# Kernel tuning notes

Hardware: AMD Instinct MI355X
Metric: run time of the kernel (lower is better)

The kernel has to match this reference:

```python
import jax, jax.numpy as jnp
import numpy as np

H = 16  # num heads
DH = 64  # head dim


def setup_inputs() -> dict:
    key = jax.random.key(0)
    ks = jax.random.split(key, 9)
    d = 1024
    s = 0.02
    return {
        "hidden_states": jax.random.normal(ks[0], (16, 1024, d), jnp.float32),
        "Wq": jax.random.normal(ks[1], (d, d), jnp.float32) * s,
        "bq": jax.random.normal(ks[2], (d,), jnp.float32) * s,
        "Wk": jax.random.normal(ks[3], (d, d), jnp.float32) * s,
        "bk": jax.random.normal(ks[4], (d,), jnp.float32) * s,
        "Wv": jax.random.normal(ks[5], (d, d), jnp.float32) * s,
        "bv": jax.random.normal(ks[6], (d,), jnp.float32) * s,
        "Wo": jax.random.normal(ks[7], (d, d), jnp.float32) * s,
        "bo": jax.random.normal(ks[8], (d,), jnp.float32) * s,
    }


def _heads(x):
    b, s, _ = x.shape
    return x.reshape(b, s, H, DH).transpose(0, 2, 1, 3)  # [B,H,S,Dh]


def reference(hidden_states, Wq, bq, Wk, bk, Wv, bv, Wo, bo):
    # torch nn.Linear: y = x @ W.T + b; weights here are [out, in]
    q = _heads(hidden_states @ Wq.T + bq)
    k = _heads(hidden_states @ Wk.T + bk)
    v = _heads(hidden_states @ Wv.T + bv)
    scores = jnp.einsum("bhqd,bhkd->bhqk", q, k) / jnp.sqrt(jnp.float32(DH))
    probs = jax.nn.softmax(scores, axis=-1)
    ctx = jnp.einsum("bhqk,bhkd->bhqd", probs, v)
    b, _, s, _ = ctx.shape
    ctx = ctx.transpose(0, 2, 1, 3).reshape(b, s, H * DH)
    out = ctx @ Wo.T + bo
    # module returns (attention_output, weights=None); return array only
    return out
```

## Files before the change

### kernel.cpp

```cpp
#include <hip/hip_runtime.h>
#include <hip/hip_bf16.h>
#include <stdint.h>


typedef short bf16x8 __attribute__((ext_vector_type(8)));
typedef float f32x4 __attribute__((ext_vector_type(4)));
typedef float f32x16 __attribute__((ext_vector_type(16)));
typedef unsigned short ushort_t;
typedef ushort_t us8 __attribute__((ext_vector_type(8)));

__device__ __forceinline__ ushort_t f2b(float f) {
    unsigned x;
    __builtin_memcpy(&x, &f, 4);
    unsigned r = (x + 0x7fffu + ((x >> 16) & 1u)) >> 16;
    return (ushort_t)r;
}

__device__ __forceinline__ void glds16(const void* g, void* l) {
    __builtin_amdgcn_global_load_lds(
        (const __attribute__((address_space(1))) void*)g,
        (__attribute__((address_space(3))) void*)l, 16, 0, 0);
}

#define MFMA16(a, b, c) __builtin_amdgcn_mfma_f32_16x16x32_bf16((a), (b), (c), 0, 0, 0)
#define MFMA32(a, b, c) __builtin_amdgcn_mfma_f32_32x32x16_bf16((a), (b), (c), 0, 0, 0)

__global__ __launch_bounds__(256, 8) void cvt4_kernel(
    const float* __restrict__ s0, const float* __restrict__ s1,
    const float* __restrict__ s2, const float* __restrict__ s3,
    ushort_t* __restrict__ d0, ushort_t* __restrict__ d1,
    ushort_t* __restrict__ d2, ushort_t* __restrict__ d3, int n8)
{
    const float* in = (blockIdx.y == 0) ? s0 : (blockIdx.y == 1) ? s1
                       : (blockIdx.y == 2) ? s2 : s3;
    ushort_t* out = (blockIdx.y == 0) ? d0 : (blockIdx.y == 1) ? d1
                       : (blockIdx.y == 2) ? d2 : d3;
    int i = blockIdx.x * 256 + threadIdx.x;
    if (i >= n8) return;
    const float4* p = (const float4*)in + (size_t)i * 2;
    float4 a = p[0], b = p[1];
    us8 v;
    v[0] = f2b(a.x); v[1] = f2b(a.y); v[2] = f2b(a.z); v[3] = f2b(a.w);
    v[4] = f2b(b.x); v[5] = f2b(b.y); v[6] = f2b(b.z); v[7] = f2b(b.w);
    *((us8*)out + i) = v;
}

__global__ __launch_bounds__(256, 8) void cvt1_kernel(
    const float* __restrict__ in, ushort_t* __restrict__ out, int n8)
{
    int i = blockIdx.x * 256 + threadIdx.x;
    if (i >= n8) return;
    const float4* p = (const float4*)in + (size_t)i * 2;
    float4 a = p[0], b = p[1];
    us8 v;
    v[0] = f2b(a.x); v[1] = f2b(a.y); v[2] = f2b(a.z); v[3] = f2b(a.w);
    v[4] = f2b(b.x); v[5] = f2b(b.y); v[6] = f2b(b.z); v[7] = f2b(b.w);
    *((us8*)out + i) = v;
}

template <bool OUTF>
__global__ __launch_bounds__(512) void gemm256_kernel(
    const ushort_t* __restrict__ A,
    const ushort_t* __restrict__ W0, const ushort_t* __restrict__ W1, const ushort_t* __restrict__ W2,
    const float* __restrict__ b0, const float* __restrict__ b1, const float* __restrict__ b2,
    void* __restrict__ C0, void* __restrict__ C1, void* __restrict__ C2,
    float s0, float s1, float s2, int N, int K)
{
    const ushort_t* W = (blockIdx.z == 0) ? W0 : ((blockIdx.z == 1) ? W1 : W2);
    const float* bias = (blockIdx.z == 0) ? b0 : ((blockIdx.z == 1) ? b1 : b2);
    void* C = (blockIdx.z == 0) ? C0 : ((blockIdx.z == 1) ? C1 : C2);
    const float scale = (blockIdx.z == 0) ? s0 : ((blockIdx.z == 1) ? s1 : s2);

    __shared__ ushort_t lds[2][4][256 * 32];

    const int tid = threadIdx.x;
    const int lane = tid & 63;
    const int wave = tid >> 6;
    const int wr = wave >> 2;
    const int wc = wave & 3;
    const int r32 = lane & 31;
    const int g = lane >> 5;

    const int gx = gridDim.x;
    const int flat = blockIdx.y * gx + blockIdx.x;
    const int cpx = (gx * gridDim.y) >> 3;
    const int swz = (flat & 7) * cpx + (flat >> 3);
    const int bm = (swz % gx) * 256;
    const int bn = (swz / gx) * 256;

    const ushort_t* Ag = A + (size_t)bm * K;
    const ushort_t* Bg = W + (size_t)bn * K;

    const int q0 = tid, q1 = 512 + tid;
    const int sr0 = q0 >> 2, sc0 = (((q0 & 3) - (sr0 >> 1)) & 3) * 8;
    const int sr1 = q1 >> 2, sc1 = (((q1 & 3) - (sr1 >> 1)) & 3) * 8;

#define STG(gbase, kcol, dst) do { \
    glds16((gbase) + (size_t)sr0 * K + (kcol) + sc0, (dst) + q0 * 8); \
    glds16((gbase) + (size_t)sr1 * K + (kcol) + sc1, (dst) + q1 * 8); } while (0)

#define BARRIER() do { \
    __builtin_amdgcn_sched_barrier(0); \
    asm volatile("s_barrier" ::: "memory"); \
    __builtin_amdgcn_sched_barrier(0); } while (0)

#define VMCNT(n) asm volatile("s_waitcnt vmcnt(" #n ")" ::: "memory")

#define ROT(r, c) (((((c) + ((r) >> 1)) & 3)) * 8)

    f32x16 acc[4][2] = {};
    bf16x8 af[2][2], bfr[2][2];

#define LDA(buf, kh, mh) do { _Pragma("unroll") \
    for (int i = 0; i < 2; ++i) { _Pragma("unroll") \
        for (int t = 0; t < 2; ++t) { \
            int row = wr * 128 + ((mh) * 2 + i) * 32 + r32; \
            af[i][t] = *(const bf16x8*)(&lds[buf][kh][0] + row * 32 + ROT(row, 2 * t + g)); \
        } } } while (0)
#define LDB(buf, kh) do { _Pragma("unroll") \
    for (int ni = 0; ni < 2; ++ni) { _Pragma("unroll") \
        for (int t = 0; t < 2; ++t) { \
            int row = wc * 64 + ni * 32 + r32; \
            bfr[ni][t] = *(const bf16x8*)(&lds[buf][2 + (kh)][0] + row * 32 + ROT(row, 2 * t + g)); \
        } } } while (0)
#define MM(mh) do { __builtin_amdgcn_s_setprio(1); _Pragma("unroll") \
    for (int i = 0; i < 2; ++i) { _Pragma("unroll") \
        for (int ni = 0; ni < 2; ++ni) { \
            acc[(mh) * 2 + i][ni] = MFMA32(af[i][0], bfr[ni][0], acc[(mh) * 2 + i][ni]); \
            acc[(mh) * 2 + i][ni] = MFMA32(af[i][1], bfr[ni][1], acc[(mh) * 2 + i][ni]); \
        } } \
    __builtin_amdgcn_s_setprio(0); } while (0)

    STG(Ag, 0,  &lds[0][0][0]);
    STG(Bg, 0,  &lds[0][2][0]);
    STG(Ag, 32, &lds[0][1][0]);
    STG(Bg, 32, &lds[0][3][0]);
    STG(Bg, 64, &lds[1][2][0]);
    STG(Ag, 64, &lds[1][0][0]);
    VMCNT(4);
    BARRIER();

#pragma unroll 1
    for (int i = 0; i < 7; ++i) {
        const int t = 2 * i;
        const int kc1 = (t + 1) * 64, kc2 = (t + 2) * 64, kc3 = (t + 3) * 64;
        LDB(0, 0); LDA(0, 0, 0);
        STG(Bg, kc1 + 32, &lds[1][3][0]);
        BARRIER(); MM(0);
        LDA(0, 0, 1);
        STG(Ag, kc1 + 32, &lds[1][1][0]);
        VMCNT(8);
        BARRIER(); MM(1);
        LDB(0, 1); LDA(0, 1, 0);
        STG(Bg, kc2, &lds[0][2][0]);
        BARRIER(); MM(0);
        LDA(0, 1, 1);
        STG(Ag, kc2, &lds[0][0][0]);
        VMCNT(8);
        BARRIER(); MM(1);
        LDB(1, 0); LDA(1, 0, 0);
        STG(Bg, kc2 + 32, &lds[0][3][0]);
        BARRIER(); MM(0);
        LDA(1, 0, 1);
        STG(Ag, kc2 + 32, &lds[0][1][0]);
        VMCNT(8);
        BARRIER(); MM(1);
        LDB(1, 1); LDA(1, 1, 0);
        STG(Bg, kc3, &lds[1][2][0]);
        BARRIER(); MM(0);
        LDA(1, 1, 1);
        STG(Ag, kc3, &lds[1][0][0]);
        VMCNT(8);
        BARRIER(); MM(1);
    }

    {
        const int kc15 = 15 * 64;
        LDB(0, 0); LDA(0, 0, 0);
        STG(Bg, kc15 + 32, &lds[1][3][0]);
        BARRIER(); MM(0);
        LDA(0, 0, 1);
        STG(Ag, kc15 + 32, &lds[1][1][0]);
        VMCNT(8);
        BARRIER(); MM(1);
        LDB(0, 1); LDA(0, 1, 0);
        BARRIER(); MM(0);
        LDA(0, 1, 1);
        VMCNT(0);
        BARRIER(); MM(1);
        LDB(1, 0); LDA(1, 0, 0); MM(0);
        LDA(1, 0, 1); MM(1);
        LDB(1, 1); LDA(1, 1, 0); MM(0);
        LDA(1, 1, 1); MM(1);
    }

#pragma unroll
    for (int ni = 0; ni < 2; ++ni) {
        const int col = bn + wc * 64 + ni * 32 + r32;
        const float bv = bias[col];
#pragma unroll
        for (int mi = 0; mi < 4; ++mi) {
            const int rbase = bm + wr * 128 + mi * 32 + 4 * g;
#pragma unroll
            for (int reg = 0; reg < 16; ++reg) {
                const int row = rbase + (reg & 3) + 8 * (reg >> 2);
                float v = (acc[mi][ni][reg] + bv) * scale;
                if (OUTF)
                    ((float*)C)[(size_t)row * N + col] = v;
                else
                    ((ushort_t*)C)[(size_t)row * N + col] = f2b(v);
            }
        }
    }
#undef STG
#undef BARRIER
#undef VMCNT
#undef ROT
#undef LDA
#undef LDB
#undef MM
}

__global__ __launch_bounds__(256, 4) void transpose_v_kernel(
    const ushort_t* __restrict__ V, ushort_t* __restrict__ Vt)
{
    __shared__ ushort_t t[64 * 65];
    const int bh = blockIdx.x;
    const int st = blockIdx.y;
    const int b = bh >> 4, h = bh & 15;
    const int tid = threadIdx.x;

#pragma unroll
    for (int i = 0; i < 16; ++i) {
        int e = i * 256 + tid;
        int s = e >> 6, d = e & 63;
        t[s * 65 + d] = V[(size_t)(b * 1024 + st * 64 + s) * 1024 + h * 64 + d];
    }
    __syncthreads();
#pragma unroll
    for (int i = 0; i < 16; ++i) {
        int e = i * 256 + tid;
        int d = e >> 6, s = e & 63;
        Vt[(size_t)(bh * 64 + d) * 1024 + st * 64 + s] = t[s * 65 + d];
    }
}

__global__ __launch_bounds__(256, 2) void attn_kernel(
    const ushort_t* __restrict__ Q, const ushort_t* __restrict__ K,
    const ushort_t* __restrict__ Vt, ushort_t* __restrict__ ctx)
{
    __shared__ ushort_t Ks[2][64 * 64];
    __shared__ ushort_t Vs[2][64 * 64];
    __shared__ ushort_t Ps[4][32 * 72];

    const int bh = blockIdx.x;
    const int qt = blockIdx.y;
    const int b = bh >> 4, h = bh & 15;
    const int tid = threadIdx.x;
    const int lane = tid & 63;
    const int wave = tid >> 6;
    const int q = lane >> 4;
    const int ml = lane & 15;

    const int cid0 = tid;
    const int cid1 = 256 + tid;
    const int r0 = cid0 >> 3, sc0 = (cid0 & 7) ^ (r0 & 7);
    const int r1 = cid1 >> 3, sc1 = (cid1 & 7) ^ (r1 & 7);
    const ushort_t* Kbase = K + (size_t)(b * 1024) * 1024 + h * 64;
    const ushort_t* Vbase = Vt + (size_t)(bh * 64) * 1024;

    bf16x8 qf[2][2];
#pragma unroll
    for (int mg = 0; mg < 2; ++mg) {
        int row = b * 1024 + qt * 128 + wave * 32 + mg * 16 + ml;
        const ushort_t* qp = Q + (size_t)row * 1024 + h * 64;
        qf[mg][0] = *(const bf16x8*)(qp + q * 8);
        qf[mg][1] = *(const bf16x8*)(qp + 32 + q * 8);
    }

    bf16x8 ones;
#pragma unroll
    for (int i = 0; i < 8; ++i) ones[i] = (short)0x3F80;

    f32x4 o[2][4] = {};
    f32x4 ls[2] = {};
    ushort_t* Pw = Ps[wave];

    glds16(Kbase + (size_t)r0 * 1024 + sc0 * 8, Ks[0] + cid0 * 8);
    glds16(Vbase + (size_t)r0 * 1024 + sc0 * 8, Vs[0] + cid0 * 8);
    glds16(Kbase + (size_t)r1 * 1024 + sc1 * 8, Ks[0] + cid1 * 8);
    glds16(Vbase + (size_t)r1 * 1024 + sc1 * 8, Vs[0] + cid1 * 8);

    for (int kt = 0; kt < 16; ++kt) {
        const int cur = kt & 1, nxt = cur ^ 1;
        __syncthreads();
        if (kt + 1 < 16) {
            const ushort_t* Kn = Kbase + (size_t)(kt + 1) * 64 * 1024;
            const ushort_t* Vn = Vbase + (kt + 1) * 64;
            glds16(Kn + (size_t)r0 * 1024 + sc0 * 8, Ks[nxt] + cid0 * 8);
            glds16(Vn + (size_t)r0 * 1024 + sc0 * 8, Vs[nxt] + cid0 * 8);
            glds16(Kn + (size_t)r1 * 1024 + sc1 * 8, Ks[nxt] + cid1 * 8);
            glds16(Vn + (size_t)r1 * 1024 + sc1 * 8, Vs[nxt] + cid1 * 8);
        }
        const ushort_t* Kc = Ks[cur];
        const ushort_t* Vc = Vs[cur];

#pragma unroll
        for (int n = 0; n < 4; ++n) {
            int row = n * 16 + ml;
            int c0 = q ^ (row & 7);
            int c1 = (4 + q) ^ (row & 7);
            bf16x8 k0 = *(const bf16x8*)(Kc + row * 64 + c0 * 8);
            bf16x8 k1 = *(const bf16x8*)(Kc + row * 64 + c1 * 8);
#pragma unroll
            for (int mg = 0; mg < 2; ++mg) {
                f32x4 z = {};
                z = MFMA16(k0, qf[mg][0], z);
                z = MFMA16(k1, qf[mg][1], z);
                float p0 = __builtin_amdgcn_exp2f(z[0]);
                float p1 = __builtin_amdgcn_exp2f(z[1]);
                float p2 = __builtin_amdgcn_exp2f(z[2]);
                float p3 = __builtin_amdgcn_exp2f(z[3]);
                __hip_bfloat162 h01 = __float22bfloat162_rn(make_float2(p0, p1));
                __hip_bfloat162 h23 = __float22bfloat162_rn(make_float2(p2, p3));
                uint2 dd;
                __builtin_memcpy(&dd.x, &h01, 4);
                __builtin_memcpy(&dd.y, &h23, 4);
                *(uint2*)(Pw + (mg * 16 + ml) * 72 + n * 16 + q * 4) = dd;
            }
        }

#pragma unroll
        for (int mg = 0; mg < 2; ++mg) {
            bf16x8 pf0 = *(const bf16x8*)(Pw + (mg * 16 + ml) * 72 + q * 8);
            bf16x8 pf1 = *(const bf16x8*)(Pw + (mg * 16 + ml) * 72 + 32 + q * 8);
            ls[mg] = MFMA16(pf0, ones, ls[mg]);
            ls[mg] = MFMA16(pf1, ones, ls[mg]);
#pragma unroll
            for (int n = 0; n < 4; ++n) {
                int row = n * 16 + ml;
                int c0 = q ^ (row & 7);
                int c1 = (4 + q) ^ (row & 7);
                bf16x8 v0 = *(const bf16x8*)(Vc + row * 64 + c0 * 8);
                bf16x8 v1 = *(const bf16x8*)(Vc + row * 64 + c1 * 8);
                o[mg][n] = MFMA16(pf0, v0, o[mg][n]);
                o[mg][n] = MFMA16(pf1, v1, o[mg][n]);
            }
        }
    }

    const int orow_base = b * 1024 + qt * 128 + wave * 32;
#pragma unroll
    for (int mg = 0; mg < 2; ++mg) {
#pragma unroll
        for (int r = 0; r < 4; ++r) {
            float lv = 1.0f / ls[mg][r];
            int orow = orow_base + mg * 16 + q * 4 + r;
#pragma unroll
            for (int n = 0; n < 4; ++n) {
                ctx[(size_t)orow * 1024 + h * 64 + n * 16 + ml] =
                    f2b(o[mg][n][r] * lv);
            }
        }
    }
}

extern "C" void kernel_launch(void* const* d_in, const int* in_sizes, int n_in,
                              void* d_out, int out_size, void* d_ws, size_t ws_size,
                              hipStream_t stream)
{
    const float* X  = (const float*)d_in[0];
    const float* Wq = (const float*)d_in[1];
    const float* bq = (const float*)d_in[2];
    const float* Wk = (const float*)d_in[3];
    const float* bk = (const float*)d_in[4];
    const float* Wv = (const float*)d_in[5];
    const float* bv = (const float*)d_in[6];
    const float* Wo = (const float*)d_in[7];
    const float* bo = (const float*)d_in[8];

    const int D = 1024;
    const int M = in_sizes[0] / D;
    const int Bb = M / 1024;
    const size_t MD = (size_t)M * D;
    const size_t DD = (size_t)D * D;

    ushort_t* ws  = (ushort_t*)d_ws;
    ushort_t* Xbf = ws;
    ushort_t* Qb  = ws + MD;
    ushort_t* Kb  = ws + 2 * MD;
    ushort_t* Vb  = ws + 3 * MD;
    ushort_t* Wqb = ws + 4 * MD;
    ushort_t* Wkb = Wqb + DD;
    ushort_t* Wvb = Wkb + DD;
    ushort_t* Wob = Wvb + DD;
    ushort_t* Vtb = Xbf;
    ushort_t* ctx = Vb;

    dim3 blk(256);
    dim3 blk512(512);

    cvt1_kernel<<<(int)(MD / 8 / 256), blk, 0, stream>>>(X, Xbf, (int)(MD / 8));
    cvt4_kernel<<<dim3((int)(DD / 8 / 256), 4), blk, 0, stream>>>(
        Wq, Wk, Wv, Wo, Wqb, Wkb, Wvb, Wob, (int)(DD / 8));

    const float qscale = 1.4426950408889634f * 0.125f;
    dim3 gqkv(M / 256, D / 256, 3);
    gemm256_kernel<false><<<gqkv, blk512, 0, stream>>>(Xbf, Wqb, Wkb, Wvb,
                                                       bq, bk, bv,
                                                       Qb, Kb, Vb,
                                                       qscale, 1.0f, 1.0f, D, D);

    transpose_v_kernel<<<dim3(Bb * 16, 16), blk, 0, stream>>>(Vb, Vtb);

    attn_kernel<<<dim3(Bb * 16, 8), blk, 0, stream>>>(Qb, Kb, Vtb, ctx);

    dim3 go(M / 256, D / 256, 1);
    gemm256_kernel<true><<<go, blk512, 0, stream>>>(ctx, Wob, Wob, Wob,
                                                    bo, bo, bo,
                                                    d_out, d_out, d_out,
                                                    1.0f, 1.0f, 1.0f, D, D);
}
```

Baseline: 398.7 us.

## Double-buffer GEMM register fragments to overlap LDS reads with MFMA

Splits the A/B register fragments of the projection GEMM into two sets (X and Y). The next half-tile's LDS reads are issued before the current MFMAs run, and the barrier moves to after the compute. Wait counts are reworked to match. The aim is to hide LDS read latency behind matrix math, at the cost of extra VGPRs and a more fragile synchronisation order across the LDS buffers.

```diff
diff --git a/kernel.cpp b/kernel.cpp
--- a/kernel.cpp
+++ b/kernel.cpp
@@ -109,25 +109,26 @@
 #define ROT(r, c) (((((c) + ((r) >> 1)) & 3)) * 8)
 
     f32x16 acc[4][2] = {};
-    bf16x8 af[2][2], bfr[2][2];
-
-#define LDA(buf, kh, mh) do { _Pragma("unroll") \
+    bf16x8 afX[2][2], bfrX[2][2];
+    bf16x8 afY[2][2], bfrY[2][2];
+
+#define LDA_(dst, buf, kh, mh) do { _Pragma("unroll") \
     for (int i = 0; i < 2; ++i) { _Pragma("unroll") \
         for (int t = 0; t < 2; ++t) { \
             int row = wr * 128 + ((mh) * 2 + i) * 32 + r32; \
-            af[i][t] = *(const bf16x8*)(&lds[buf][kh][0] + row * 32 + ROT(row, 2 * t + g)); \
+            dst[i][t] = *(const bf16x8*)(&lds[buf][kh][0] + row * 32 + ROT(row, 2 * t + g)); \
         } } } while (0)
-#define LDB(buf, kh) do { _Pragma("unroll") \
+#define LDB_(dst, buf, kh) do { _Pragma("unroll") \
     for (int ni = 0; ni < 2; ++ni) { _Pragma("unroll") \
         for (int t = 0; t < 2; ++t) { \
             int row = wc * 64 + ni * 32 + r32; \
-            bfr[ni][t] = *(const bf16x8*)(&lds[buf][2 + (kh)][0] + row * 32 + ROT(row, 2 * t + g)); \
+            dst[ni][t] = *(const bf16x8*)(&lds[buf][2 + (kh)][0] + row * 32 + ROT(row, 2 * t + g)); \
         } } } while (0)
-#define MM(mh) do { __builtin_amdgcn_s_setprio(1); _Pragma("unroll") \
+#define MM_(a, b, mh) do { __builtin_amdgcn_s_setprio(1); _Pragma("unroll") \
     for (int i = 0; i < 2; ++i) { _Pragma("unroll") \
         for (int ni = 0; ni < 2; ++ni) { \
-            acc[(mh) * 2 + i][ni] = MFMA32(af[i][0], bfr[ni][0], acc[(mh) * 2 + i][ni]); \
-            acc[(mh) * 2 + i][ni] = MFMA32(af[i][1], bfr[ni][1], acc[(mh) * 2 + i][ni]); \
+            acc[(mh) * 2 + i][ni] = MFMA32(a[i][0], b[ni][0], acc[(mh) * 2 + i][ni]); \
+            acc[(mh) * 2 + i][ni] = MFMA32(a[i][1], b[ni][1], acc[(mh) * 2 + i][ni]); \
         } } \
     __builtin_amdgcn_s_setprio(0); } while (0)
 
@@ -139,59 +140,64 @@
     STG(Ag, 64, &lds[1][0][0]);
     VMCNT(4);
     BARRIER();
+    LDA_(afX, 0, 0, 0); LDB_(bfrX, 0, 0);
 
 #pragma unroll 1
     for (int i = 0; i < 7; ++i) {
         const int t = 2 * i;
         const int kc1 = (t + 1) * 64, kc2 = (t + 2) * 64, kc3 = (t + 3) * 64;
-        LDB(0, 0); LDA(0, 0, 0);
+        LDA_(afY, 0, 0, 1); LDB_(bfrY, 0, 0);
         STG(Bg, kc1 + 32, &lds[1][3][0]);
-        BARRIER(); MM(0);
-        LDA(0, 0, 1);
+        VMCNT(6);
+        MM_(afX, bfrX, 0); BARRIER();
+        LDA_(afX, 0, 1, 0); LDB_(bfrX, 0, 1);
         STG(Ag, kc1 + 32, &lds[1][1][0]);
-        VMCNT(8);
-        BARRIER(); MM(1);
-        LDB(0, 1); LDA(0, 1, 0);
+        MM_(afY, bfrY, 1); BARRIER();
+        LDA_(afY, 0, 1, 1); LDB_(bfrY, 0, 1);
         STG(Bg, kc2, &lds[0][2][0]);
-        BARRIER(); MM(0);
-        LDA(0, 1, 1);
+        VMCNT(6);
+        MM_(afX, bfrX, 0); BARRIER();
+        LDA_(afX, 1, 0, 0); LDB_(bfrX, 1, 0);
         STG(Ag, kc2, &lds[0][0][0]);
-        VMCNT(8);
-        BARRIER(); MM(1);
-        LDB(1, 0); LDA(1, 0, 0);
+        MM_(afY, bfrY, 1); BARRIER();
+        LDA_(afY, 1, 0, 1); LDB_(bfrY, 1, 0);
         STG(Bg, kc2 + 32, &lds[0][3][0]);
-        BARRIER(); MM(0);
-        LDA(1, 0, 1);
+        VMCNT(6);
+        MM_(afX, bfrX, 0); BARRIER();
+        LDA_(afX, 1, 1, 0); LDB_(bfrX, 1, 1);
         STG(Ag, kc2 + 32, &lds[0][1][0]);
-        VMCNT(8);
-        BARRIER(); MM(1);
-        LDB(1, 1); LDA(1, 1, 0);
+        MM_(afY, bfrY, 1); BARRIER();
+        LDA_(afY, 1, 1, 1); LDB_(bfrY, 1, 1);
         STG(Bg, kc3, &lds[1][2][0]);
-        BARRIER(); MM(0);
-        LDA(1, 1, 1);
+        VMCNT(6);
+        MM_(afX, bfrX, 0); BARRIER();
+        LDA_(afX, 0, 0, 0); LDB_(bfrX, 0, 0);
         STG(Ag, kc3, &lds[1][0][0]);
-        VMCNT(8);
-        BARRIER(); MM(1);
+        MM_(afY, bfrY, 1); BARRIER();
     }
 
     {
         const int kc15 = 15 * 64;
-        LDB(0, 0); LDA(0, 0, 0);
+        LDA_(afY, 0, 0, 1); LDB_(bfrY, 0, 0);
         STG(Bg, kc15 + 32, &lds[1][3][0]);
-        BARRIER(); MM(0);
-        LDA(0, 0, 1);
+        VMCNT(6);
+        MM_(afX, bfrX, 0); BARRIER();
+        LDA_(afX, 0, 1, 0); LDB_(bfrX, 0, 1);
         STG(Ag, kc15 + 32, &lds[1][1][0]);
-        VMCNT(8);
-        BARRIER(); MM(1);
-        LDB(0, 1); LDA(0, 1, 0);
-        BARRIER(); MM(0);
-        LDA(0, 1, 1);
+        MM_(afY, bfrY, 1); BARRIER();
+        LDA_(afY, 0, 1, 1); LDB_(bfrY, 0, 1);
+        VMCNT(6);
+        MM_(afX, bfrX, 0); BARRIER();
+        LDA_(afX, 1, 0, 0); LDB_(bfrX, 1, 0);
+        MM_(afY, bfrY, 1); BARRIER();
+        LDA_(afY, 1, 0, 1); LDB_(bfrY, 1, 0);
         VMCNT(0);
-        BARRIER(); MM(1);
-        LDB(1, 0); LDA(1, 0, 0); MM(0);
-        LDA(1, 0, 1); MM(1);
-        LDB(1, 1); LDA(1, 1, 0); MM(0);
-        LDA(1, 1, 1); MM(1);
+        MM_(afX, bfrX, 0); BARRIER();
+        LDA_(afX, 1, 1, 0); LDB_(bfrX, 1, 1);
+        MM_(afY, bfrY, 1);
+        LDA_(afY, 1, 1, 1); LDB_(bfrY, 1, 1);
+        MM_(afX, bfrX, 0);
+        MM_(afY, bfrY, 1);
     }
 
 #pragma unroll
@@ -216,9 +222,9 @@
 #undef BARRIER
 #undef VMCNT
 #undef ROT
-#undef LDA
-#undef LDB
-#undef MM
+#undef LDA_
+#undef LDB_
+#undef MM_
 }
 
 __global__ __launch_bounds__(256, 4) void transpose_v_kernel(
```

Measured after the change: 403.1 us. No clear change (+1.1%).
